# Kernel tuning notes

Hardware: AMD Instinct MI355X
Metric: run time of the kernel (lower is better)

## Reference

```python
import math
import jax, jax.numpy as jnp
import numpy as np

NUM_EXPERTS = 8
TOP_K = 2
CAPACITY_FACTOR = 1.0
B, S, H, I = 4, 2048, 1024, 4096


def setup_inputs() -> dict:
    key = jax.random.key(0)
    k_x, k_rw, k_wi, k_wo = jax.random.split(key, 4)
    x = jax.random.normal(k_x, (B, S, H), dtype=jnp.float32)
    # router: nn.Linear(H, E), xavier_uniform weight, zero-ish bias
    lim = math.sqrt(6.0 / (H + NUM_EXPERTS))
    router_w = jax.random.uniform(k_rw, (NUM_EXPERTS, H), minval=-lim, maxval=lim, dtype=jnp.float32)
    router_b = jnp.zeros((NUM_EXPERTS,), dtype=jnp.float32)
    # expert weights (scaled randn for numerical sanity)
    experts_inter = jax.random.normal(k_wi, (NUM_EXPERTS - 1, H, I), dtype=jnp.float32) / math.sqrt(H)
    experts_out = jax.random.normal(k_wo, (NUM_EXPERTS - 1, I, H), dtype=jnp.float32) / math.sqrt(I)
    return {"x": x, "router_w": router_w, "router_b": router_b,
            "experts_inter": experts_inter, "experts_out": experts_out}


def reference(x, router_w, router_b, experts_inter, experts_out):
    batch, seq, hidden = x.shape
    n_exp = router_w.shape[0]
    n_tok = batch * seq
    cap = math.ceil(n_tok / n_exp * CAPACITY_FACTOR)  # expert capacity

    # router: linear + softmax
    logits = jnp.einsum('bsh,eh->bse', x, router_w) + router_b
    weights_flat = jax.nn.softmax(logits, axis=-1).reshape(n_tok, n_exp)
    x_flat = x.reshape(n_tok, hidden)

    # top-k gating; scatter topk values back into a dense [N, E] matrix
    topk_vals, topk_idx = jax.lax.top_k(weights_flat, TOP_K)
    rows = jnp.arange(n_tok)[:, None]
    topk_flat = jnp.zeros_like(weights_flat).at[rows, topk_idx].set(topk_vals)
    routing_mask = (topk_flat > 0).astype(jnp.int32)

    # no-op path = last expert column (identity * gate weight)
    noop_w = topk_flat[:, -1]
    noop_mask = routing_mask[:, -1].astype(x.dtype)

    # real experts: columns 0..E-2; capacity-limited dispatch via per-column sort
    expert_w = topk_flat[:, :-1]           # [N, E-1]
    expert_mask = routing_mask[:, :-1]     # [N, E-1]
    sorted_indices = jnp.argsort(-expert_mask, axis=0)[:cap]          # [cap, E-1]
    sorted_mask = jnp.take_along_axis(expert_mask, sorted_indices, axis=0)
    used_idx = (sorted_indices * sorted_mask).reshape(-1)             # masked -> index 0

    inputs = x_flat[used_idx] * sorted_mask.reshape(-1).astype(x.dtype)[:, None]
    inputs = inputs.reshape(cap, n_exp - 1, hidden)                   # [cap, E-1, H]
    in_w = jnp.take_along_axis(expert_w, sorted_indices, axis=0)      # [cap, E-1]

    # batched per-expert FFN
    h = jax.nn.relu(jnp.einsum('ceh,ehi->cei', inputs, experts_inter))
    out = jnp.einsum('cei,eih->ceh', h, experts_out) * in_w[..., None]

    # scatter-combine (masked slots write zeros into row 0, harmless)
    combined = jnp.zeros_like(x_flat).at[used_idx].add(out.reshape(-1, hidden))
    combined = combined + x_flat * (noop_w * noop_mask)[:, None]
    return combined.reshape(batch, seq, hidden)
```

## Files before the change

### kernel.cpp

```cpp
#include <hip/hip_runtime.h>
#include <hip/hip_bf16.h>
#include <stdint.h>
#include <stddef.h>


#define N_TOK   8192
#define HDIM    1024
#define IDIM    4096
#define NEXP    7
#define CAP     1024

typedef __bf16 bf16_t;
typedef bf16_t bf16x8 __attribute__((ext_vector_type(8)));
typedef float  f32x4  __attribute__((ext_vector_type(4)));

typedef __attribute__((address_space(3))) char lds_char_t;
typedef __attribute__((address_space(1))) const char glob_char_t;

__device__ __forceinline__ void load_lds16(const void* g, void* l) {
    __builtin_amdgcn_global_load_lds((glob_char_t*)(uintptr_t)g,
                                     (lds_char_t*)(uintptr_t)l, 16, 0, 0);
}

__device__ __forceinline__ bf16x8 pack8(const float* v) {
    bf16x8 r;
#pragma unroll
    for (int j = 0; j < 8; j++) r[j] = (bf16_t)v[j];
    return r;
}

__global__ __launch_bounds__(256) void router_kernel(
    const float* __restrict__ x, const float* __restrict__ rw,
    const float* __restrict__ rb, float* __restrict__ routew)
{
    const int wave = threadIdx.x >> 6, lane = threadIdx.x & 63;
    const int t = blockIdx.x * 4 + wave;
    const float4* xr = (const float4*)(x + (size_t)t * HDIM);
    float4 xv[4];
#pragma unroll
    for (int r = 0; r < 4; r++) xv[r] = xr[lane + r * 64];
    float p[8];
#pragma unroll
    for (int e = 0; e < 8; e++) {
        const float4* wr = (const float4*)(rw + (size_t)e * HDIM);
        float s = 0.f;
#pragma unroll
        for (int r = 0; r < 4; r++) {
            float4 wv = wr[lane + r * 64];
            s += xv[r].x * wv.x + xv[r].y * wv.y + xv[r].z * wv.z + xv[r].w * wv.w;
        }
#pragma unroll
        for (int o = 32; o; o >>= 1) s += __shfl_xor(s, o, 64);
        p[e] = s + rb[e];
    }
    float m = p[0];
#pragma unroll
    for (int e = 1; e < 8; e++) m = fmaxf(m, p[e]);
    float sum = 0.f;
#pragma unroll
    for (int e = 0; e < 8; e++) { p[e] = expf(p[e] - m); sum += p[e]; }
    float inv = 1.f / sum;
#pragma unroll
    for (int e = 0; e < 8; e++) p[e] *= inv;
    int i1 = 0;
#pragma unroll
    for (int e = 1; e < 8; e++) if (p[e] > p[i1]) i1 = e;
    int i2 = (i1 == 0) ? 1 : 0;
#pragma unroll
    for (int e = 0; e < 8; e++) if (e != i1 && p[e] > p[i2]) i2 = e;
    if (lane == 0) {
#pragma unroll
        for (int c = 0; c < 8; c++)
            routew[(size_t)t * 8 + c] = (c == i1) ? p[i1] : ((c == i2) ? p[i2] : 0.f);
    }
}

__global__ __launch_bounds__(1024) void compact_kernel(
    const float* __restrict__ routew, int* __restrict__ list,
    float* __restrict__ wsel)
{
    const int tid = threadIdx.x, wave = tid >> 6, lane = tid & 63;
    for (int i = tid; i < NEXP * CAP; i += 1024) { list[i] = -1; wsel[i] = 0.f; }
    __syncthreads();
    __shared__ int cnt[16][NEXP];
    int base[NEXP];
#pragma unroll
    for (int e = 0; e < NEXP; e++) base[e] = 0;
    const unsigned long long below = (lane == 63) ? ~0ull >> 1 : ((1ull << lane) - 1);
    for (int chunk = 0; chunk < N_TOK / 1024; chunk++) {
        const int t = chunk * 1024 + tid;
        float w[NEXP]; bool sel[NEXP]; int rnk[NEXP]; int wtot[NEXP];
#pragma unroll
        for (int e = 0; e < NEXP; e++) {
            w[e] = routew[(size_t)t * 8 + e];
            sel[e] = (w[e] > 0.f);
            unsigned long long mask = __ballot(sel[e]);
            rnk[e] = __popcll(mask & below);
            wtot[e] = __popcll(mask);
        }
        if (lane == 0) {
#pragma unroll
            for (int e = 0; e < NEXP; e++) cnt[wave][e] = wtot[e];
        }
        __syncthreads();
#pragma unroll
        for (int e = 0; e < NEXP; e++) {
            int pre = base[e];
            for (int w2 = 0; w2 < wave; w2++) pre += cnt[w2][e];
            int rank = pre + rnk[e];
            if (sel[e] && rank < CAP) {
                list[e * CAP + rank] = t;
                wsel[e * CAP + rank] = w[e];
            }
            int tot = 0;
            for (int w2 = 0; w2 < 16; w2++) tot += cnt[w2][e];
            base[e] += tot;
        }
        __syncthreads();
    }
}

__global__ __launch_bounds__(128) void gather_kernel(
    const float* __restrict__ x, const int* __restrict__ list,
    bf16_t* __restrict__ A)
{
    const int row = blockIdx.x;
    const int t = list[row];
    const int i = threadIdx.x;
    float4 v0 = {0.f, 0.f, 0.f, 0.f}, v1 = v0;
    if (t >= 0) {
        const float4* xs = (const float4*)(x + (size_t)t * HDIM);
        v0 = xs[i * 2];
        v1 = xs[i * 2 + 1];
    }
    bf16x8 o;
    o[0] = (bf16_t)v0.x; o[1] = (bf16_t)v0.y; o[2] = (bf16_t)v0.z; o[3] = (bf16_t)v0.w;
    o[4] = (bf16_t)v1.x; o[5] = (bf16_t)v1.y; o[6] = (bf16_t)v1.z; o[7] = (bf16_t)v1.w;
    ((bf16x8*)(A + (size_t)row * HDIM))[i] = o;
}

__global__ __launch_bounds__(256) void initout_kernel(
    const float* __restrict__ x, const float* __restrict__ routew,
    float* __restrict__ out)
{
    const int t = blockIdx.x;
    const float c = routew[(size_t)t * 8 + 7];
    const float4* xs = (const float4*)(x + (size_t)t * HDIM);
    float4* o = (float4*)(out + (size_t)t * HDIM);
    float4 v = xs[threadIdx.x];
    v.x *= c; v.y *= c; v.z *= c; v.w *= c;
    o[threadIdx.x] = v;
}

template<int KDIM, int NDIM, bool IS_G1>
__global__ __launch_bounds__(256) void ffn_gemm(
    const bf16_t* __restrict__ Ab, const float* __restrict__ Wb,
    bf16_t* __restrict__ Hout, const int* __restrict__ list,
    const float* __restrict__ wsel, float* __restrict__ out)
{
    constexpr int BM = 128, BN = 128, BK = 32;
    __shared__ __align__(16) bf16_t As[BM * BK];
    __shared__ __align__(16) bf16_t Bs[BN * BK];
    const int tid = threadIdx.x, wave = tid >> 6, lane = tid & 63;
    const int e = blockIdx.z, mblk = blockIdx.y * BM, nblk = blockIdx.x * BN;

    const bf16_t* Ae = Ab + ((size_t)e * CAP + mblk) * KDIM;
    const float*  We = Wb + (size_t)e * KDIM * NDIM + nblk;

    const int ar = tid >> 2, ac = (tid & 3) * 8;
    const bf16_t* ag0 = Ae + (size_t)ar * KDIM + ac;
    const bf16_t* ag1 = ag0 + (size_t)64 * KDIM;
    bf16_t* as0 = As + wave * 512;
    bf16_t* as1 = As + 2048 + wave * 512;

    const int bn = tid & 127, bc = (tid >> 7) * 2;
    const float* bg = We + bn;
    bf16_t* bsw0 = Bs + bn * BK + ((bc ^ (bn & 3)) * 8);
    bf16_t* bsw1 = Bs + bn * BK + (((bc + 1) ^ (bn & 3)) * 8);

    const int wm = (wave & 1) * 64, wn = (wave >> 1) * 64;
    const int lr = lane & 15, q = lane >> 4;
    const int sw = q ^ ((wn + lr) & 3);

    f32x4 acc[4][4] = {};

    for (int k0 = 0; k0 < KDIM; k0 += BK) {
        load_lds16(ag0 + k0, as0);
        load_lds16(ag1 + k0, as1);
        const float* bp = bg + (size_t)(k0 + bc * 8) * NDIM;
        float v[16];
#pragma unroll
        for (int j = 0; j < 16; j++) v[j] = bp[(size_t)j * NDIM];
        bf16x8 p0 = pack8(v), p1 = pack8(v + 8);
        *(bf16x8*)bsw0 = p0;
        *(bf16x8*)bsw1 = p1;
        __syncthreads();
        bf16x8 af[4], bfr[4];
#pragma unroll
        for (int i = 0; i < 4; i++)
            af[i] = *(const bf16x8*)(As + (wm + i * 16 + lr) * BK + q * 8);
#pragma unroll
        for (int j = 0; j < 4; j++)
            bfr[j] = *(const bf16x8*)(Bs + (wn + j * 16 + lr) * BK + sw * 8);
#pragma unroll
        for (int i = 0; i < 4; i++)
#pragma unroll
            for (int j = 0; j < 4; j++)
                acc[i][j] = __builtin_amdgcn_mfma_f32_16x16x32_bf16(af[i], bfr[j], acc[i][j], 0, 0, 0);
        __syncthreads();
    }

    if (IS_G1) {
        bf16_t* Ho = Hout + ((size_t)e * CAP + mblk) * NDIM + nblk;
#pragma unroll
        for (int i = 0; i < 4; i++) {
            const int r0 = wm + i * 16 + q * 4;
#pragma unroll
            for (int reg = 0; reg < 4; reg++) {
                bf16_t* row = Ho + (size_t)(r0 + reg) * NDIM;
#pragma unroll
                for (int j = 0; j < 4; j++)
                    row[wn + j * 16 + lr] = (bf16_t)fmaxf(acc[i][j][reg], 0.f);
            }
        }
    } else {
#pragma unroll
        for (int i = 0; i < 4; i++) {
            const int r0 = mblk + wm + i * 16 + q * 4;
#pragma unroll
            for (int reg = 0; reg < 4; reg++) {
                const int row = r0 + reg;
                const int tok = list[e * CAP + row];
                const float wgt = wsel[e * CAP + row];
                if (tok >= 0) {
                    float* orow = out + (size_t)tok * NDIM + nblk;
#pragma unroll
                    for (int j = 0; j < 4; j++)
                        atomicAdd(orow + wn + j * 16 + lr, acc[i][j][reg] * wgt);
                }
            }
        }
    }
}

extern "C" void kernel_launch(void* const* d_in, const int* in_sizes, int n_in,
                              void* d_out, int out_size, void* d_ws, size_t ws_size,
                              hipStream_t stream) {
    const float* x  = (const float*)d_in[0];
    const float* rw = (const float*)d_in[1];
    const float* rb = (const float*)d_in[2];
    const float* w1 = (const float*)d_in[3];
    const float* w2 = (const float*)d_in[4];
    float* out = (float*)d_out;

    char* ws = (char*)d_ws;
    float*  routew = (float*)(ws);
    int*    list   = (int*)(ws + 262144);
    float*  wsel   = (float*)(ws + 262144 + 28672);
    bf16_t* Abuf   = (bf16_t*)(ws + 319488);
    bf16_t* Hbuf   = (bf16_t*)(ws + 319488 + 14680064);

    router_kernel<<<N_TOK / 4, 256, 0, stream>>>(x, rw, rb, routew);
    compact_kernel<<<1, 1024, 0, stream>>>(routew, list, wsel);
    gather_kernel<<<NEXP * CAP, 128, 0, stream>>>(x, list, Abuf);
    initout_kernel<<<N_TOK, 256, 0, stream>>>(x, routew, out);
    ffn_gemm<HDIM, IDIM, true><<<dim3(IDIM / 128, CAP / 128, NEXP), 256, 0, stream>>>(
        Abuf, w1, Hbuf, nullptr, nullptr, nullptr);
    ffn_gemm<IDIM, HDIM, false><<<dim3(HDIM / 128, CAP / 128, NEXP), 256, 0, stream>>>(
        Hbuf, w2, nullptr, list, wsel, out);
}
```

Baseline: 611.7 us.

## Pre-transpose expert weights to bf16 and use direct-to-LDS GEMM with split-K

Adds a kernel that transposes and converts each expert's fp32 weights to bf16 K-major layout in workspace before each GEMM. The GEMM can then load B tiles straight into LDS with global_load_lds instead of converting fp32 in-kernel. The second GEMM is split along K into two halves with atomic accumulation to raise the block count. It also parallelises capacity compaction across experts, one block per expert. The cost is an extra pass over the weights on every call plus more workspace; the old path is kept as a fallback when workspace is too small.

After: 551.7 us. -9.8%, faster.

```diff
diff --git a/kernel.cpp b/kernel.cpp
--- a/kernel.cpp
+++ b/kernel.cpp
@@ -79,43 +79,28 @@
     const float* __restrict__ routew, int* __restrict__ list,
     float* __restrict__ wsel)
 {
+    const int e = blockIdx.x;
     const int tid = threadIdx.x, wave = tid >> 6, lane = tid & 63;
-    for (int i = tid; i < NEXP * CAP; i += 1024) { list[i] = -1; wsel[i] = 0.f; }
+    for (int i = tid; i < CAP; i += 1024) { list[e * CAP + i] = -1; wsel[e * CAP + i] = 0.f; }
+    __shared__ int cnt[16];
     __syncthreads();
-    __shared__ int cnt[16][NEXP];
-    int base[NEXP];
-#pragma unroll
-    for (int e = 0; e < NEXP; e++) base[e] = 0;
+    int base = 0;
     const unsigned long long below = (lane == 63) ? ~0ull >> 1 : ((1ull << lane) - 1);
     for (int chunk = 0; chunk < N_TOK / 1024; chunk++) {
         const int t = chunk * 1024 + tid;
-        float w[NEXP]; bool sel[NEXP]; int rnk[NEXP]; int wtot[NEXP];
-#pragma unroll
-        for (int e = 0; e < NEXP; e++) {
-            w[e] = routew[(size_t)t * 8 + e];
-            sel[e] = (w[e] > 0.f);
-            unsigned long long mask = __ballot(sel[e]);
-            rnk[e] = __popcll(mask & below);
-            wtot[e] = __popcll(mask);
-        }
-        if (lane == 0) {
-#pragma unroll
-            for (int e = 0; e < NEXP; e++) cnt[wave][e] = wtot[e];
-        }
-        __syncthreads();
-#pragma unroll
-        for (int e = 0; e < NEXP; e++) {
-            int pre = base[e];
-            for (int w2 = 0; w2 < wave; w2++) pre += cnt[w2][e];
-            int rank = pre + rnk[e];
-            if (sel[e] && rank < CAP) {
-                list[e * CAP + rank] = t;
-                wsel[e * CAP + rank] = w[e];
-            }
-            int tot = 0;
-            for (int w2 = 0; w2 < 16; w2++) tot += cnt[w2][e];
-            base[e] += tot;
-        }
+        const float w = routew[(size_t)t * 8 + e];
+        const bool sel = (w > 0.f);
+        const unsigned long long mask = __ballot(sel);
+        const int rnk = __popcll(mask & below);
+        if (lane == 0) cnt[wave] = __popcll(mask);
+        __syncthreads();
+        int pre = base;
+        for (int w2 = 0; w2 < wave; w2++) pre += cnt[w2];
+        const int rank = pre + rnk;
+        if (sel && rank < CAP) { list[e * CAP + rank] = t; wsel[e * CAP + rank] = w; }
+        int tot = 0;
+        for (int w2 = 0; w2 < 16; w2++) tot += cnt[w2];
+        base += tot;
         __syncthreads();
     }
 }
@@ -152,8 +137,126 @@
     o[threadIdx.x] = v;
 }
 
+template<int K, int N>
+__global__ __launch_bounds__(256) void transpose_cvt(
+    const float* __restrict__ W, bf16_t* __restrict__ Wt)
+{
+    __shared__ float Ts[64][65];
+    const int t = threadIdx.x;
+    const int e = blockIdx.z;
+    const int ktile = blockIdx.y * 64, ntile = blockIdx.x * 64;
+    const float* We = W + (size_t)e * K * N;
+    const int kr = t >> 4, nc = (t & 15) * 4;
+#pragma unroll
+    for (int j = 0; j < 4; j++) {
+        const float4 v = *(const float4*)(We + (size_t)(ktile + kr + j * 16) * N + ntile + nc);
+        Ts[nc + 0][kr + j * 16] = v.x;
+        Ts[nc + 1][kr + j * 16] = v.y;
+        Ts[nc + 2][kr + j * 16] = v.z;
+        Ts[nc + 3][kr + j * 16] = v.w;
+    }
+    __syncthreads();
+    const int n = t >> 2, kc = (t & 3) * 16;
+    bf16_t* o = Wt + ((size_t)e * N + ntile + n) * K + ktile + kc;
+    bf16x8 p0, p1;
+#pragma unroll
+    for (int i = 0; i < 8; i++) {
+        p0[i] = (bf16_t)Ts[n][kc + i];
+        p1[i] = (bf16_t)Ts[n][kc + 8 + i];
+    }
+    ((bf16x8*)o)[0] = p0;
+    ((bf16x8*)o)[1] = p1;
+}
+
+template<int KDIM, int NDIM, int KSPLIT, bool IS_G1>
+__global__ __launch_bounds__(256) void ffn_gemm_t(
+    const bf16_t* __restrict__ Ab, const bf16_t* __restrict__ Bt,
+    bf16_t* __restrict__ Hout, const int* __restrict__ list,
+    const float* __restrict__ wsel, float* __restrict__ out)
+{
+    constexpr int BM = 128, BN = 128, BK = 32;
+    constexpr int KLEN = KDIM / KSPLIT;
+    __shared__ __align__(16) bf16_t As[BM * BK];
+    __shared__ __align__(16) bf16_t Bs[BN * BK];
+    const int tid = threadIdx.x, wave = tid >> 6;
+    const int lane = tid & 63;
+    const int e = blockIdx.z / KSPLIT, ks = blockIdx.z % KSPLIT;
+    const int mblk = blockIdx.y * BM, nblk = blockIdx.x * BN;
+
+    const bf16_t* Ae = Ab + ((size_t)e * CAP + mblk) * KDIM + (size_t)ks * KLEN;
+    const bf16_t* Be = Bt + ((size_t)e * NDIM + nblk) * KDIM + (size_t)ks * KLEN;
+
+    const int r = tid >> 2, c = (tid & 3) * 8;
+    const bf16_t* ag0 = Ae + (size_t)r * KDIM + c;
+    const bf16_t* ag1 = ag0 + (size_t)64 * KDIM;
+    const bf16_t* bg0 = Be + (size_t)r * KDIM + c;
+    const bf16_t* bg1 = bg0 + (size_t)64 * KDIM;
+    bf16_t* as0 = As + wave * 512;
+    bf16_t* as1 = As + 2048 + wave * 512;
+    bf16_t* bs0 = Bs + wave * 512;
+    bf16_t* bs1 = Bs + 2048 + wave * 512;
+
+    const int wm = (wave & 1) * 64, wn = (wave >> 1) * 64;
+    const int lr = lane & 15, q = lane >> 4;
+
+    f32x4 acc[4][4] = {};
+
+    for (int k0 = 0; k0 < KLEN; k0 += BK) {
+        load_lds16(ag0 + k0, as0);
+        load_lds16(ag1 + k0, as1);
+        load_lds16(bg0 + k0, bs0);
+        load_lds16(bg1 + k0, bs1);
+        __syncthreads();
+        bf16x8 af[4], bfr[4];
+#pragma unroll
+        for (int i = 0; i < 4; i++)
+            af[i] = *(const bf16x8*)(As + (wm + i * 16 + lr) * BK + q * 8);
+#pragma unroll
+        for (int j = 0; j < 4; j++)
+            bfr[j] = *(const bf16x8*)(Bs + (wn + j * 16 + lr) * BK + q * 8);
+#pragma unroll
+        for (int i = 0; i < 4; i++)
+#pragma unroll
+            for (int j = 0; j < 4; j++)
+                acc[i][j] = __builtin_amdgcn_mfma_f32_16x16x32_bf16(af[i], bfr[j], acc[i][j], 0, 0, 0);
+        __syncthreads();
+    }
+
+    if (IS_G1) {
+        bf16_t* Ho = Hout + ((size_t)e * CAP + mblk) * NDIM + nblk;
+#pragma unroll
+        for (int i = 0; i < 4; i++) {
+            const int r0 = wm + i * 16 + q * 4;
+#pragma unroll
+            for (int reg = 0; reg < 4; reg++) {
+                bf16_t* row = Ho + (size_t)(r0 + reg) * NDIM;
+#pragma unroll
+                for (int j = 0; j < 4; j++)
+                    row[wn + j * 16 + lr] = (bf16_t)fmaxf(acc[i][j][reg], 0.f);
+            }
+        }
+    } else {
+#pragma unroll
+        for (int i = 0; i < 4; i++) {
+            const int r0 = mblk + wm + i * 16 + q * 4;
+#pragma unroll
+            for (int reg = 0; reg < 4; reg++) {
+                const int row = r0 + reg;
+                const int tok = list[e * CAP + row];
+                const float wgt = wsel[e * CAP + row];
+                if (tok >= 0) {
+                    float* orow = out + (size_t)tok * NDIM + nblk;
+#pragma unroll
+                    for (int j = 0; j < 4; j++)
+                        atomicAdd(orow + wn + j * 16 + lr, acc[i][j][reg] * wgt);
+                }
+            }
+        }
+    }
+}
+
 template<int KDIM, int NDIM, bool IS_G1>
-__global__ __launch_bounds__(256) void ffn_gemm(
+__global__ __launch_bounds__(256) void ffn_gemm_fused(
     const bf16_t* __restrict__ Ab, const float* __restrict__ Wb,
     bf16_t* __restrict__ Hout, const int* __restrict__ list,
     const float* __restrict__ wsel, float* __restrict__ out)
@@ -258,14 +361,27 @@
     int*    list   = (int*)(ws + 262144);
     float*  wsel   = (float*)(ws + 262144 + 28672);
     bf16_t* Abuf   = (bf16_t*)(ws + 319488);
-    bf16_t* Hbuf   = (bf16_t*)(ws + 319488 + 14680064);
+    bf16_t* Hbuf   = (bf16_t*)(ws + 14999552);
+    bf16_t* Wt     = (bf16_t*)(ws + 73719808);
+
+    const size_t NEED = 73719808ull + 58720256ull;
 
     router_kernel<<<N_TOK / 4, 256, 0, stream>>>(x, rw, rb, routew);
-    compact_kernel<<<1, 1024, 0, stream>>>(routew, list, wsel);
+    compact_kernel<<<NEXP, 1024, 0, stream>>>(routew, list, wsel);
     gather_kernel<<<NEXP * CAP, 128, 0, stream>>>(x, list, Abuf);
     initout_kernel<<<N_TOK, 256, 0, stream>>>(x, routew, out);
-    ffn_gemm<HDIM, IDIM, true><<<dim3(IDIM / 128, CAP / 128, NEXP), 256, 0, stream>>>(
-        Abuf, w1, Hbuf, nullptr, nullptr, nullptr);
-    ffn_gemm<IDIM, HDIM, false><<<dim3(HDIM / 128, CAP / 128, NEXP), 256, 0, stream>>>(
-        Hbuf, w2, nullptr, list, wsel, out);
-}
+
+    if (ws_size >= NEED) {
+        transpose_cvt<HDIM, IDIM><<<dim3(IDIM / 64, HDIM / 64, NEXP), 256, 0, stream>>>(w1, Wt);
+        ffn_gemm_t<HDIM, IDIM, 1, true><<<dim3(IDIM / 128, CAP / 128, NEXP), 256, 0, stream>>>(
+            Abuf, Wt, Hbuf, nullptr, nullptr, nullptr);
+        transpose_cvt<IDIM, HDIM><<<dim3(HDIM / 64, IDIM / 64, NEXP), 256, 0, stream>>>(w2, Wt);
+        ffn_gemm_t<IDIM, HDIM, 2, false><<<dim3(HDIM / 128, CAP / 128, NEXP * 2), 256, 0, stream>>>(
+            Hbuf, Wt, nullptr, list, wsel, out);
+    } else {
+        ffn_gemm_fused<HDIM, IDIM, true><<<dim3(IDIM / 128, CAP / 128, NEXP), 256, 0, stream>>>(
+            Abuf, w1, Hbuf, nullptr, nullptr, nullptr);
+        ffn_gemm_fused<IDIM, HDIM, false><<<dim3(HDIM / 128, CAP / 128, NEXP), 256, 0, stream>>>(
+            Hbuf, w2, nullptr, list, wsel, out);
+    }
+}
```
